# Kernel tuning notes

Hardware: AMD Instinct MI355X
Metric: run time of the kernel (lower is better)

The kernel has to match this reference:

```python
import jax, jax.numpy as jnp
import numpy as np

DELTA = -5.0
DECAY = 0.95
EPS = 1e-05


def setup_inputs() -> dict:
    key = jax.random.key(0)
    k1, k2, k3 = jax.random.split(key, 3)
    N, K, D = 16384, 1024, 256
    z = jax.random.normal(k1, (N, D), dtype=jnp.float32)
    centroids = jax.random.normal(k2, (K, D), dtype=jnp.float32)
    ema_w = jax.random.normal(k3, (K, D), dtype=jnp.float32)
    ema_cluster_size = jnp.ones((K,), dtype=jnp.float32)
    return {"z": z, "centroids": centroids, "ema_w": ema_w,
            "ema_cluster_size": ema_cluster_size}


def reference(z, centroids, ema_w, ema_cluster_size):
    # z: [N, D]; centroids/ema_w: [K, D]; ema_cluster_size: [K]
    K = centroids.shape[0]
    # squared L2 distances via ||z||^2 - 2 z.C^T + ||c||^2 (same math as
    # sum((z[:,None,:]-C)**2, -1), without the (N,K,D) intermediate)
    z_sq = jnp.sum(z * z, axis=1, keepdims=True)          # [N, 1]
    c_sq = jnp.sum(centroids * centroids, axis=1)         # [K]
    z_dist = z_sq - 2.0 * (z @ centroids.T) + c_sq        # [N, K]
    gamma = jax.nn.softmax(DELTA * z_dist, axis=1)        # [N, K]
    idx = jnp.argmax(gamma, axis=1)                       # [N] int
    # recons = one_hot(idx) @ centroids == gather
    recons = centroids[idx]                               # [N, D]
    # --- EMA codebook update (training branch), expressed purely ---
    counts = jnp.zeros((K,), dtype=z.dtype).at[idx].add(jnp.ones((), z.dtype))
    new_cs = ema_cluster_size * DECAY + (1.0 - DECAY) * counts
    n = jnp.sum(new_cs)
    new_cs = (new_cs + EPS) / (n + K * EPS) * n
    dw = jax.ops.segment_sum(z, idx, num_segments=K)      # == Idx.T @ z, [K, D]
    new_w = ema_w * DECAY + (1.0 - DECAY) * dw
    new_centroids = new_w / new_cs[:, None]
    # straight-through estimator
    recons = z + jax.lax.stop_gradient(recons - z)
    return recons, gamma, new_centroids
```

## Files before the change

kernel.cpp:

```cpp
#include <hip/hip_runtime.h>


#define DECAY 0.95f
#define OMD   0.05f
#define EPSV  1e-5f

using i32x4  = __attribute__((ext_vector_type(4))) int;
using i32x16 = __attribute__((ext_vector_type(16))) int;

typedef __attribute__((address_space(3))) unsigned int       lds_uint;
typedef const __attribute__((address_space(1))) unsigned int glb_uint;

__device__ __forceinline__ void gload16(const void* g, const void* l) {
  __builtin_amdgcn_global_load_lds((glb_uint*)(unsigned long long)g,
                                   (lds_uint*)(unsigned int)(unsigned long long)l,
                                   16, 0, 0);
}

__global__ __launch_bounds__(256) void prep(const float* __restrict__ z,
                                            const float* __restrict__ cent,
                                            const float* __restrict__ ema_cs,
                                            signed char* __restrict__ z8,
                                            signed char* __restrict__ c8,
                                            float* __restrict__ sz,
                                            float* __restrict__ sc,
                                            float* __restrict__ csq,
                                            float* __restrict__ dwzero,
                                            float* __restrict__ S) {
  const int bid = blockIdx.x;
  const int t   = threadIdx.x;
  if (bid < 2176) {
    const bool isz = bid < 2048;
    const float* src = isz ? z : cent;
    const int rb = isz ? bid : (bid - 2048);
    const int r  = rb * 8 + (t >> 5);
    const int d0 = (t & 31) * 8;
    const float4 a = *(const float4*)&src[(size_t)r * 256 + d0];
    const float4 b = *(const float4*)&src[(size_t)r * 256 + d0 + 4];
    float f[8] = {a.x, a.y, a.z, a.w, b.x, b.y, b.z, b.w};
    float am = 0.f, ssq = 0.f;
#pragma unroll
    for (int j = 0; j < 8; ++j) { am = fmaxf(am, fabsf(f[j])); ssq += f[j] * f[j]; }
#pragma unroll
    for (int off = 16; off; off >>= 1) {
      am  = fmaxf(am, __shfl_down(am, off, 32));
      ssq += __shfl_down(ssq, off, 32);
    }
    am = __shfl(am, 0, 32);
    const float s  = fmaxf(am, 1e-6f) * (1.0f / 127.0f);
    const float rs = 1.0f / s;
    union { signed char c[8]; uint2 u; } H, L;
#pragma unroll
    for (int j = 0; j < 8; ++j) {
      float q = rintf(f[j] * rs);
      q = fminf(fmaxf(q, -127.f), 127.f);
      H.c[j] = (signed char)(int)q;
      float res = f[j] - q * s;
      float lq = rintf(res * rs * 256.0f);
      lq = fminf(fmaxf(lq, -127.f), 127.f);
      L.c[j] = (signed char)(int)lq;
    }
    signed char* dst = (isz ? z8 : c8) + (size_t)r * 512 + (d0 >> 6) * 128 + (d0 & 63);
    *(uint2*)dst        = H.u;
    *(uint2*)(dst + 64) = L.u;
    if ((t & 31) == 0) {
      if (isz) sz[r] = s;
      else { sc[r] = s; csq[r] = ssq; }
    }
  } else if (bid < 2433) {
    const int i = (bid - 2176) * 256 + t;
    ((float4*)dwzero)[i] = (float4){0.f, 0.f, 0.f, 0.f};
  } else {
    float s = ema_cs[t] + ema_cs[t + 256] + ema_cs[t + 512] + ema_cs[t + 768];
#pragma unroll
    for (int off = 32; off; off >>= 1) s += __shfl_down(s, off);
    __shared__ float wsum[4];
    if ((t & 63) == 0) wsum[t >> 6] = s;
    __syncthreads();
    if (t == 0) S[0] = wsum[0] + wsum[1] + wsum[2] + wsum[3];
  }
}

__global__ __launch_bounds__(256, 2) void dist_gemm_i8(
    const signed char* __restrict__ z8, const signed char* __restrict__ c8,
    const float* __restrict__ sz, const float* __restrict__ sc,
    const float* __restrict__ csq, float* __restrict__ dist) {
  __shared__ signed char lds[2][128 * 128];

  const int tid  = threadIdx.x;
  const int lane = tid & 63;
  const int w    = tid >> 6;

  const int bid = blockIdx.x;
  const int lin = (bid & 7) * 128 + (bid >> 3);
  const int m0  = (lin >> 3) * 128;
  const int n0  = (lin & 7) * 128;

  const int wm0 = (w >> 1) * 64;
  const int wn0 = (w & 1) * 64;

  i32x16 accA[2][2];
  i32x16 accB[2][2];
#pragma unroll
  for (int i = 0; i < 2; ++i)
#pragma unroll
    for (int j = 0; j < 2; ++j) {
      accA[i][j] = (i32x16)(0);
      accB[i][j] = (i32x16)(0);
    }

  const int srow = lane >> 3;
  const int scb  = lane & 7;

  for (int kk = 0; kk < 4; ++kk) {
    __syncthreads();
#pragma unroll
    for (int j = 0; j < 4; ++j) {
      const int r0    = w * 32 + j * 8;
      const int row   = r0 + srow;
      const int chunk = scb ^ (row & 7);
      gload16(z8 + (size_t)(m0 + row) * 512 + kk * 128 + chunk * 16, &lds[0][r0 * 128]);
      gload16(c8 + (size_t)(n0 + row) * 512 + kk * 128 + chunk * 16, &lds[1][r0 * 128]);
    }
    __syncthreads();
#pragma unroll
    for (int s = 0; s < 2; ++s) {
      i32x4 ah[2], al[2], bh[2], bl[2];
      const int kc = s * 2 + (lane >> 5);
#pragma unroll
      for (int fi = 0; fi < 2; ++fi) {
        const int ra = wm0 + fi * 32 + (lane & 31);
        ah[fi] = *(const i32x4*)&lds[0][ra * 128 + ((kc)     ^ (ra & 7)) * 16];
        al[fi] = *(const i32x4*)&lds[0][ra * 128 + ((kc + 4) ^ (ra & 7)) * 16];
        const int rb = wn0 + fi * 32 + (lane & 31);
        bh[fi] = *(const i32x4*)&lds[1][rb * 128 + ((kc)     ^ (rb & 7)) * 16];
        bl[fi] = *(const i32x4*)&lds[1][rb * 128 + ((kc + 4) ^ (rb & 7)) * 16];
      }
#pragma unroll
      for (int i = 0; i < 2; ++i)
#pragma unroll
        for (int j = 0; j < 2; ++j) {
          accA[i][j] = __builtin_amdgcn_mfma_i32_32x32x32_i8(ah[i], bh[j], accA[i][j], 0, 0, 0);
          accB[i][j] = __builtin_amdgcn_mfma_i32_32x32x32_i8(ah[i], bl[j], accB[i][j], 0, 0, 0);
          accB[i][j] = __builtin_amdgcn_mfma_i32_32x32x32_i8(al[i], bh[j], accB[i][j], 0, 0, 0);
        }
    }
  }

#pragma unroll
  for (int j = 0; j < 2; ++j) {
    const int colb = n0 + wn0 + j * 32 + (lane & 31);
    const float scv = sc[colb];
    const float cqv = csq[colb];
#pragma unroll
    for (int i = 0; i < 2; ++i) {
#pragma unroll
      for (int reg = 0; reg < 16; ++reg) {
        const int row = m0 + wm0 + i * 32 + (reg & 3) + 8 * (reg >> 2) + 4 * (lane >> 5);
        const float dotv = (float)accA[i][j][reg] + (float)accB[i][j][reg] * (1.0f / 256.0f);
        dist[(size_t)row * 1024 + colb] = cqv - 2.0f * sz[row] * scv * dotv;
      }
    }
  }
}

__global__ __launch_bounds__(256) void row_softmax(const float* __restrict__ z,
                                                   const float* __restrict__ cent,
                                                   float* __restrict__ gamma,
                                                   float* __restrict__ recons,
                                                   float* __restrict__ dw,
                                                   float* __restrict__ counts,
                                                   int K) {
  const int n = blockIdx.x;
  const int t = threadIdx.x;
  float* row = gamma + (size_t)n * K;
  const float4 s = ((const float4*)row)[t];

  float mv = s.x; int mi = 4 * t;
  if (s.y < mv) { mv = s.y; mi = 4 * t + 1; }
  if (s.z < mv) { mv = s.z; mi = 4 * t + 2; }
  if (s.w < mv) { mv = s.w; mi = 4 * t + 3; }

#pragma unroll
  for (int off = 32; off; off >>= 1) {
    const float ov = __shfl_down(mv, off);
    const int   oi = __shfl_down(mi, off);
    if (ov < mv || (ov == mv && oi < mi)) { mv = ov; mi = oi; }
  }

  __shared__ float wv[4];
  __shared__ int   wi[4];
  __shared__ float fmin_s;
  __shared__ int   fidx_s;
  __shared__ float fsum_s;
  const int wave = t >> 6;
  if ((t & 63) == 0) { wv[wave] = mv; wi[wave] = mi; }
  __syncthreads();
  if (t == 0) {
    float bv = wv[0]; int bi = wi[0];
#pragma unroll
    for (int wq = 1; wq < 4; ++wq)
      if (wv[wq] < bv || (wv[wq] == bv && wi[wq] < bi)) { bv = wv[wq]; bi = wi[wq]; }
    fmin_s = bv; fidx_s = bi;
  }
  __syncthreads();

  const float bm = fmin_s;
  const float e0 = __expf(-5.0f * (s.x - bm));
  const float e1 = __expf(-5.0f * (s.y - bm));
  const float e2 = __expf(-5.0f * (s.z - bm));
  const float e3 = __expf(-5.0f * (s.w - bm));
  float ls = e0 + e1 + e2 + e3;
#pragma unroll
  for (int off = 32; off; off >>= 1) ls += __shfl_down(ls, off);
  if ((t & 63) == 0) wv[wave] = ls;
  __syncthreads();
  if (t == 0) fsum_s = wv[0] + wv[1] + wv[2] + wv[3];
  __syncthreads();

  const float inv = 1.0f / fsum_s;
  float4 g;
  g.x = e0 * inv; g.y = e1 * inv; g.z = e2 * inv; g.w = e3 * inv;
  ((float4*)row)[t] = g;

  const int idx = fidx_s;
  const float zv = z[(size_t)n * 256 + t];
  recons[(size_t)n * 256 + t] = cent[(size_t)idx * 256 + t];
  atomicAdd(&dw[(size_t)idx * 256 + t], zv);
  if (t == 0) atomicAdd(&counts[idx], 1.0f);
}

__global__ __launch_bounds__(256) void finalize(const float* __restrict__ ema_w,
                                                const float* __restrict__ ema_cs,
                                                const float* __restrict__ counts,
                                                const float* __restrict__ dw,
                                                const float* __restrict__ S,
                                                float* __restrict__ outc,
                                                float fN) {
  const int k = blockIdx.x;
  const int t = threadIdx.x;
  const float n   = DECAY * S[0] + OMD * fN;
  const float v   = DECAY * ema_cs[k] + OMD * counts[k];
  const float ncs = (v + EPSV) / (n + 1024.0f * EPSV) * n;
  const size_t i  = (size_t)k * 256 + t;
  outc[i] = (DECAY * ema_w[i] + OMD * dw[i]) / ncs;
}

extern "C" void kernel_launch(void* const* d_in, const int* in_sizes, int n_in,
                              void* d_out, int out_size, void* d_ws, size_t ws_size,
                              hipStream_t stream) {
  const float* z      = (const float*)d_in[0];
  const float* cent   = (const float*)d_in[1];
  const float* ema_w  = (const float*)d_in[2];
  const float* ema_cs = (const float*)d_in[3];

  const int K = in_sizes[3];
  const int D = in_sizes[1] / K;
  const int N = in_sizes[0] / D;

  float* out    = (float*)d_out;
  float* recons = out;
  float* gamma  = out + (size_t)N * D;
  float* outc   = gamma + (size_t)N * K;

  signed char* z8 = (signed char*)recons;
  signed char* c8 = (signed char*)outc;
  float* sz = outc + (size_t)K * 512 / 4;
  float* sc = sz + N;

  float* dw     = (float*)d_ws;
  float* counts = dw + (size_t)K * D;
  float* csq    = counts + K;
  float* S      = csq + K;

  prep<<<2434, 256, 0, stream>>>(z, cent, ema_cs, z8, c8, sz, sc, csq, dw, S);

  dist_gemm_i8<<<(N / 128) * (K / 128), 256, 0, stream>>>(z8, c8, sz, sc, csq, gamma);

  row_softmax<<<N, 256, 0, stream>>>(z, cent, gamma, recons, dw, counts, K);

  finalize<<<K, 256, 0, stream>>>(ema_w, ema_cs, counts, dw, S, outc, (float)N);
}
```

Measured before the change: 77.67 us.

## Fuse z quantization, distance GEMM, softmax and scatter into one kernel

Replaces the separate z-quantization, int8 distance GEMM and row-softmax kernels with one fused kernel per 64-row block. The block quantizes z directly into LDS and runs the GEMM twice over all centroids. The first pass computes per-row min, argmin and partial exp sums, and the second recomputes distances and writes normalized gamma directly. This avoids writing and rereading the full N×K distance matrix and the z8 buffer in global memory, at the cost of doing the GEMM twice. It also drops to 128 blocks of 64 rows, which may limit occupancy and parallelism.

```diff
diff --git a/kernel.cpp b/kernel.cpp
--- a/kernel.cpp
+++ b/kernel.cpp
@@ -17,26 +17,20 @@
                                    16, 0, 0);
 }
 
-__global__ __launch_bounds__(256) void prep(const float* __restrict__ z,
-                                            const float* __restrict__ cent,
+__global__ __launch_bounds__(256) void prep(const float* __restrict__ cent,
                                             const float* __restrict__ ema_cs,
-                                            signed char* __restrict__ z8,
                                             signed char* __restrict__ c8,
-                                            float* __restrict__ sz,
                                             float* __restrict__ sc,
                                             float* __restrict__ csq,
                                             float* __restrict__ dwzero,
                                             float* __restrict__ S) {
   const int bid = blockIdx.x;
   const int t   = threadIdx.x;
-  if (bid < 2176) {
-    const bool isz = bid < 2048;
-    const float* src = isz ? z : cent;
-    const int rb = isz ? bid : (bid - 2048);
-    const int r  = rb * 8 + (t >> 5);
+  if (bid < 128) {
+    const int r  = bid * 8 + (t >> 5);
     const int d0 = (t & 31) * 8;
-    const float4 a = *(const float4*)&src[(size_t)r * 256 + d0];
-    const float4 b = *(const float4*)&src[(size_t)r * 256 + d0 + 4];
+    const float4 a = *(const float4*)&cent[(size_t)r * 256 + d0];
+    const float4 b = *(const float4*)&cent[(size_t)r * 256 + d0 + 4];
     float f[8] = {a.x, a.y, a.z, a.w, b.x, b.y, b.z, b.w};
     float am = 0.f, ssq = 0.f;
 #pragma unroll
@@ -60,15 +54,12 @@
       lq = fminf(fmaxf(lq, -127.f), 127.f);
       L.c[j] = (signed char)(int)lq;
     }
-    signed char* dst = (isz ? z8 : c8) + (size_t)r * 512 + (d0 >> 6) * 128 + (d0 & 63);
+    signed char* dst = c8 + (size_t)r * 512 + (d0 >> 6) * 128 + (d0 & 63);
     *(uint2*)dst        = H.u;
     *(uint2*)(dst + 64) = L.u;
-    if ((t & 31) == 0) {
-      if (isz) sz[r] = s;
-      else { sc[r] = s; csq[r] = ssq; }
-    }
-  } else if (bid < 2433) {
-    const int i = (bid - 2176) * 256 + t;
+    if ((t & 31) == 0) { sc[r] = s; csq[r] = ssq; }
+  } else if (bid < 385) {
+    const int i = (bid - 128) * 256 + t;
     ((float4*)dwzero)[i] = (float4){0.f, 0.f, 0.f, 0.f};
   } else {
     float s = ema_cs[t] + ema_cs[t + 256] + ema_cs[t + 512] + ema_cs[t + 768];
@@ -81,153 +72,186 @@
   }
 }
 
-__global__ __launch_bounds__(256, 2) void dist_gemm_i8(
-    const signed char* __restrict__ z8, const signed char* __restrict__ c8,
-    const float* __restrict__ sz, const float* __restrict__ sc,
-    const float* __restrict__ csq, float* __restrict__ dist) {
-  __shared__ signed char lds[2][128 * 128];
-
-  const int tid  = threadIdx.x;
-  const int lane = tid & 63;
-  const int w    = tid >> 6;
-
-  const int bid = blockIdx.x;
-  const int lin = (bid & 7) * 128 + (bid >> 3);
-  const int m0  = (lin >> 3) * 128;
-  const int n0  = (lin & 7) * 128;
-
-  const int wm0 = (w >> 1) * 64;
-  const int wn0 = (w & 1) * 64;
-
-  i32x16 accA[2][2];
-  i32x16 accB[2][2];
-#pragma unroll
-  for (int i = 0; i < 2; ++i)
-#pragma unroll
-    for (int j = 0; j < 2; ++j) {
-      accA[i][j] = (i32x16)(0);
-      accB[i][j] = (i32x16)(0);
-    }
-
-  const int srow = lane >> 3;
-  const int scb  = lane & 7;
-
-  for (int kk = 0; kk < 4; ++kk) {
-    __syncthreads();
-#pragma unroll
-    for (int j = 0; j < 4; ++j) {
-      const int r0    = w * 32 + j * 8;
-      const int row   = r0 + srow;
-      const int chunk = scb ^ (row & 7);
-      gload16(z8 + (size_t)(m0 + row) * 512 + kk * 128 + chunk * 16, &lds[0][r0 * 128]);
-      gload16(c8 + (size_t)(n0 + row) * 512 + kk * 128 + chunk * 16, &lds[1][r0 * 128]);
-    }
-    __syncthreads();
-#pragma unroll
-    for (int s = 0; s < 2; ++s) {
-      i32x4 ah[2], al[2], bh[2], bl[2];
-      const int kc = s * 2 + (lane >> 5);
-#pragma unroll
-      for (int fi = 0; fi < 2; ++fi) {
-        const int ra = wm0 + fi * 32 + (lane & 31);
-        ah[fi] = *(const i32x4*)&lds[0][ra * 128 + ((kc)     ^ (ra & 7)) * 16];
-        al[fi] = *(const i32x4*)&lds[0][ra * 128 + ((kc + 4) ^ (ra & 7)) * 16];
-        const int rb = wn0 + fi * 32 + (lane & 31);
-        bh[fi] = *(const i32x4*)&lds[1][rb * 128 + ((kc)     ^ (rb & 7)) * 16];
-        bl[fi] = *(const i32x4*)&lds[1][rb * 128 + ((kc + 4) ^ (rb & 7)) * 16];
-      }
-#pragma unroll
-      for (int i = 0; i < 2; ++i)
-#pragma unroll
-        for (int j = 0; j < 2; ++j) {
-          accA[i][j] = __builtin_amdgcn_mfma_i32_32x32x32_i8(ah[i], bh[j], accA[i][j], 0, 0, 0);
-          accB[i][j] = __builtin_amdgcn_mfma_i32_32x32x32_i8(ah[i], bl[j], accB[i][j], 0, 0, 0);
-          accB[i][j] = __builtin_amdgcn_mfma_i32_32x32x32_i8(al[i], bh[j], accB[i][j], 0, 0, 0);
-        }
-    }
-  }
-
-#pragma unroll
-  for (int j = 0; j < 2; ++j) {
-    const int colb = n0 + wn0 + j * 32 + (lane & 31);
-    const float scv = sc[colb];
-    const float cqv = csq[colb];
-#pragma unroll
-    for (int i = 0; i < 2; ++i) {
-#pragma unroll
-      for (int reg = 0; reg < 16; ++reg) {
-        const int row = m0 + wm0 + i * 32 + (reg & 3) + 8 * (reg >> 2) + 4 * (lane >> 5);
-        const float dotv = (float)accA[i][j][reg] + (float)accB[i][j][reg] * (1.0f / 256.0f);
-        dist[(size_t)row * 1024 + colb] = cqv - 2.0f * sz[row] * scv * dotv;
-      }
-    }
-  }
-}
-
-__global__ __launch_bounds__(256) void row_softmax(const float* __restrict__ z,
-                                                   const float* __restrict__ cent,
-                                                   float* __restrict__ gamma,
-                                                   float* __restrict__ recons,
-                                                   float* __restrict__ dw,
-                                                   float* __restrict__ counts,
-                                                   int K) {
-  const int n = blockIdx.x;
-  const int t = threadIdx.x;
-  float* row = gamma + (size_t)n * K;
-  const float4 s = ((const float4*)row)[t];
-
-  float mv = s.x; int mi = 4 * t;
-  if (s.y < mv) { mv = s.y; mi = 4 * t + 1; }
-  if (s.z < mv) { mv = s.z; mi = 4 * t + 2; }
-  if (s.w < mv) { mv = s.w; mi = 4 * t + 3; }
-
-#pragma unroll
-  for (int off = 32; off; off >>= 1) {
-    const float ov = __shfl_down(mv, off);
-    const int   oi = __shfl_down(mi, off);
-    if (ov < mv || (ov == mv && oi < mi)) { mv = ov; mi = oi; }
-  }
-
-  __shared__ float wv[4];
-  __shared__ int   wi[4];
-  __shared__ float fmin_s;
-  __shared__ int   fidx_s;
-  __shared__ float fsum_s;
-  const int wave = t >> 6;
-  if ((t & 63) == 0) { wv[wave] = mv; wi[wave] = mi; }
-  __syncthreads();
-  if (t == 0) {
-    float bv = wv[0]; int bi = wi[0];
-#pragma unroll
-    for (int wq = 1; wq < 4; ++wq)
-      if (wv[wq] < bv || (wv[wq] == bv && wi[wq] < bi)) { bv = wv[wq]; bi = wi[wq]; }
-    fmin_s = bv; fidx_s = bi;
+#define STAGE(u, buf) do {                                                   \
+    const int ct_ = (u) >> 2, kk_ = (u) & 3;                                 \
+    _Pragma("unroll")                                                        \
+    for (int rnd = 0; rnd < 4; ++rnd) {                                      \
+      const int cl_ = w * 32 + rnd * 8 + (lane >> 3);                        \
+      const int p_  = lane & 7;                                              \
+      gload16(c8 + (size_t)(ct_ * 128 + cl_) * 512 + kk_ * 128 +             \
+                  ((p_ ^ (cl_ & 7)) * 16),                                   \
+              &lB[buf][(w * 32 + rnd * 8) * 128]);                           \
+    }                                                                        \
+  } while (0)
+
+__global__ __launch_bounds__(256, 2) void fused_vq(
+    const float* __restrict__ z, const float* __restrict__ cent,
+    const signed char* __restrict__ c8, const float* __restrict__ sc,
+    const float* __restrict__ csq, float* __restrict__ gamma,
+    float* __restrict__ recons, float* __restrict__ dw,
+    float* __restrict__ counts) {
+  __shared__ signed char lA[64 * 512];
+  __shared__ signed char lB[2][128 * 128];
+  __shared__ float sMv[16][64];
+  __shared__ float sSv[16][64];
+  __shared__ int   sIv[16][64];
+  __shared__ float fM[64];
+  __shared__ float fInv[64];
+  __shared__ int   fIdx[64];
+  __shared__ float sZs[64];
+
+  const int t = threadIdx.x, lane = t & 63, w = t >> 6;
+  const int hi = lane >> 5, l31 = lane & 31;
+  const int wr = w >> 1, wc = w & 1;
+  const int m0 = blockIdx.x * 64;
+
+  {
+    const int c  = lane;
+    const int kk = c >> 4, ch = (c & 15) >> 2, jb = (c & 3) * 4;
+#pragma unroll 1
+    for (int it = 0; it < 16; ++it) {
+      const int r = it * 4 + w;
+      const float4 v = *(const float4*)&z[(size_t)(m0 + r) * 256 + c * 4];
+      float am = fmaxf(fmaxf(fabsf(v.x), fabsf(v.y)), fmaxf(fabsf(v.z), fabsf(v.w)));
+#pragma unroll
+      for (int off = 32; off; off >>= 1) am = fmaxf(am, __shfl_xor(am, off));
+      const float s  = fmaxf(am, 1e-6f) * (1.0f / 127.0f);
+      const float rs = 1.0f / s;
+      const float f[4] = {v.x, v.y, v.z, v.w};
+      unsigned int hw = 0, lw = 0;
+#pragma unroll
+      for (int j = 0; j < 4; ++j) {
+        float q = rintf(f[j] * rs);
+        q = fminf(fmaxf(q, -127.f), 127.f);
+        float res = f[j] - q * s;
+        float lq = rintf(res * rs * 256.0f);
+        lq = fminf(fmaxf(lq, -127.f), 127.f);
+        hw |= ((unsigned int)(unsigned char)(signed char)(int)q)  << (8 * j);
+        lw |= ((unsigned int)(unsigned char)(signed char)(int)lq) << (8 * j);
+      }
+      const int haddr = r * 512 + kk * 128 + ((ch ^ (r & 7)) * 16) + jb;
+      *(unsigned int*)&lA[haddr]      = hw;
+      *(unsigned int*)&lA[haddr ^ 64] = lw;
+      if (lane == 0) sZs[r] = s;
+    }
   }
   __syncthreads();
 
-  const float bm = fmin_s;
-  const float e0 = __expf(-5.0f * (s.x - bm));
-  const float e1 = __expf(-5.0f * (s.y - bm));
-  const float e2 = __expf(-5.0f * (s.z - bm));
-  const float e3 = __expf(-5.0f * (s.w - bm));
-  float ls = e0 + e1 + e2 + e3;
-#pragma unroll
-  for (int off = 32; off; off >>= 1) ls += __shfl_down(ls, off);
-  if ((t & 63) == 0) wv[wave] = ls;
-  __syncthreads();
-  if (t == 0) fsum_s = wv[0] + wv[1] + wv[2] + wv[3];
-  __syncthreads();
-
-  const float inv = 1.0f / fsum_s;
-  float4 g;
-  g.x = e0 * inv; g.y = e1 * inv; g.z = e2 * inv; g.w = e3 * inv;
-  ((float4*)row)[t] = g;
-
-  const int idx = fidx_s;
-  const float zv = z[(size_t)n * 256 + t];
-  recons[(size_t)n * 256 + t] = cent[(size_t)idx * 256 + t];
-  atomicAdd(&dw[(size_t)idx * 256 + t], zv);
-  if (t == 0) atomicAdd(&counts[idx], 1.0f);
+  float szv[16];
+#pragma unroll
+  for (int reg = 0; reg < 16; ++reg)
+    szv[reg] = sZs[wr * 32 + (reg & 3) + 8 * (reg >> 2) + 4 * hi];
+
+  const int ra = wr * 32 + l31;
+
+  i32x16 accA[2], accB[2];
+
+#pragma unroll 1
+  for (int pass = 0; pass < 2; ++pass) {
+    STAGE(0, 0);
+#pragma unroll 1
+    for (int u = 0; u < 32; ++u) {
+      const int cur = u & 1;
+      const int ct = u >> 2, kk = u & 3;
+      if (kk == 0) {
+        accA[0] = (i32x16)(0); accA[1] = (i32x16)(0);
+        accB[0] = (i32x16)(0); accB[1] = (i32x16)(0);
+      }
+      __syncthreads();
+      if (u + 1 < 32) STAGE(u + 1, cur ^ 1);
+#pragma unroll
+      for (int s = 0; s < 2; ++s) {
+        const int kc = s * 2 + hi;
+        const i32x4 ah = *(const i32x4*)&lA[ra * 512 + kk * 128 + ((kc ^ (ra & 7)) * 16)];
+        const i32x4 al = *(const i32x4*)&lA[ra * 512 + kk * 128 + (((kc + 4) ^ (ra & 7)) * 16)];
+#pragma unroll
+        for (int fj = 0; fj < 2; ++fj) {
+          const int rb = wc * 64 + fj * 32 + l31;
+          const i32x4 bh = *(const i32x4*)&lB[cur][rb * 128 + ((kc ^ (rb & 7)) * 16)];
+          const i32x4 bl = *(const i32x4*)&lB[cur][rb * 128 + (((kc + 4) ^ (rb & 7)) * 16)];
+          accA[fj] = __builtin_amdgcn_mfma_i32_32x32x32_i8(ah, bh, accA[fj], 0, 0, 0);
+          accB[fj] = __builtin_amdgcn_mfma_i32_32x32x32_i8(ah, bl, accB[fj], 0, 0, 0);
+          accB[fj] = __builtin_amdgcn_mfma_i32_32x32x32_i8(al, bh, accB[fj], 0, 0, 0);
+        }
+      }
+      if (kk == 3) {
+        const int cg0 = ct * 128 + wc * 64 + l31;
+        const float sc0 = sc[cg0],      cq0 = csq[cg0];
+        const float sc1 = sc[cg0 + 32], cq1 = csq[cg0 + 32];
+        if (pass == 0) {
+#pragma unroll
+          for (int reg = 0; reg < 16; ++reg) {
+            const float d0 = (float)accA[0][reg] + (float)accB[0][reg] * (1.0f / 256.0f);
+            const float d1 = (float)accA[1][reg] + (float)accB[1][reg] * (1.0f / 256.0f);
+            const float s0 = cq0 - 2.0f * szv[reg] * sc0 * d0;
+            const float s1 = cq1 - 2.0f * szv[reg] * sc1 * d1;
+            float mv; int mi;
+            if (s1 < s0) { mv = s1; mi = cg0 + 32; } else { mv = s0; mi = cg0; }
+#pragma unroll
+            for (int off = 16; off; off >>= 1) {
+              const float ov = __shfl_xor(mv, off);
+              const int   oi = __shfl_xor(mi, off);
+              if (ov < mv || (ov == mv && oi < mi)) { mv = ov; mi = oi; }
+            }
+            float e = __expf(-5.0f * (s0 - mv)) + __expf(-5.0f * (s1 - mv));
+#pragma unroll
+            for (int off = 16; off; off >>= 1) e += __shfl_xor(e, off);
+            if (l31 == 0) {
+              const int rl = wr * 32 + (reg & 3) + 8 * (reg >> 2) + 4 * hi;
+              sMv[ct * 2 + wc][rl] = mv;
+              sSv[ct * 2 + wc][rl] = e;
+              sIv[ct * 2 + wc][rl] = mi;
+            }
+          }
+        } else {
+#pragma unroll
+          for (int reg = 0; reg < 16; ++reg) {
+            const int rl = wr * 32 + (reg & 3) + 8 * (reg >> 2) + 4 * hi;
+            const float d0 = (float)accA[0][reg] + (float)accB[0][reg] * (1.0f / 256.0f);
+            const float d1 = (float)accA[1][reg] + (float)accB[1][reg] * (1.0f / 256.0f);
+            const float s0 = cq0 - 2.0f * szv[reg] * sc0 * d0;
+            const float s1 = cq1 - 2.0f * szv[reg] * sc1 * d1;
+            const float m = fM[rl], inv = fInv[rl];
+            gamma[(size_t)(m0 + rl) * 1024 + cg0]      = __expf(-5.0f * (s0 - m)) * inv;
+            gamma[(size_t)(m0 + rl) * 1024 + cg0 + 32] = __expf(-5.0f * (s1 - m)) * inv;
+          }
+        }
+      }
+    }
+    if (pass == 0) {
+      __syncthreads();
+      if (t < 64) {
+        float m = 3.0e38f; int mi = 0;
+#pragma unroll
+        for (int e = 0; e < 16; ++e) {
+          const float me = sMv[e][t];
+          if (me < m) { m = me; mi = sIv[e][t]; }
+        }
+        float sum = 0.f;
+#pragma unroll
+        for (int e = 0; e < 16; ++e)
+          sum += sSv[e][t] * __expf(-5.0f * (sMv[e][t] - m));
+        fM[t] = m; fInv[t] = 1.0f / sum; fIdx[t] = mi;
+        atomicAdd(&counts[mi], 1.0f);
+      }
+      __syncthreads();
+    }
+  }
+
+#pragma unroll 1
+  for (int it = 0; it < 16; ++it) {
+    const int r = it * 4 + w;
+    const int n = m0 + r;
+    const int idx = fIdx[r];
+    const float4 zv = *(const float4*)&z[(size_t)n * 256 + lane * 4];
+    const float4 cv = *(const float4*)&cent[(size_t)idx * 256 + lane * 4];
+    *(float4*)&recons[(size_t)n * 256 + lane * 4] = cv;
+    float* dp = &dw[(size_t)idx * 256 + lane * 4];
+    atomicAdd(dp + 0, zv.x);
+    atomicAdd(dp + 1, zv.y);
+    atomicAdd(dp + 2, zv.z);
+    atomicAdd(dp + 3, zv.w);
+  }
 }
 
 __global__ __launch_bounds__(256) void finalize(const float* __restrict__ ema_w,
@@ -263,21 +287,17 @@
   float* gamma  = out + (size_t)N * D;
   float* outc   = gamma + (size_t)N * K;
 
-  signed char* z8 = (signed char*)recons;
   signed char* c8 = (signed char*)outc;
-  float* sz = outc + (size_t)K * 512 / 4;
-  float* sc = sz + N;
+  float* sc = (float*)((char*)outc + (size_t)K * 512);
 
   float* dw     = (float*)d_ws;
   float* counts = dw + (size_t)K * D;
   float* csq    = counts + K;
   float* S      = csq + K;
 
-  prep<<<2434, 256, 0, stream>>>(z, cent, ema_cs, z8, c8, sz, sc, csq, dw, S);
-
-  dist_gemm_i8<<<(N / 128) * (K / 128), 256, 0, stream>>>(z8, c8, sz, sc, csq, gamma);
-
-  row_softmax<<<N, 256, 0, stream>>>(z, cent, gamma, recons, dw, counts, K);
+  prep<<<386, 256, 0, stream>>>(cent, ema_cs, c8, sc, csq, dw, S);
+
+  fused_vq<<<N / 64, 256, 0, stream>>>(z, cent, c8, sc, csq, gamma, recons, dw, counts);
 
   finalize<<<K, 256, 0, stream>>>(ema_w, ema_cs, counts, dw, S, outc, (float)N);
 }
```

After: 285.2 us. 3.67x slower.

## Fuse softmax into int8 distance GEMM using two-pass recompute with partial stats

Applied to the files above, without the earlier changes.

The distance GEMM now runs twice. The first pass produces per-row partial min, argmin and exp-sum statistics for each 64-column slice. A small merge kernel combines these into the final max, the inverse sum and the index. The second pass recomputes the distances and writes the normalized gamma directly. This avoids writing the full NxK distance matrix and reading it back for the row softmax, at the cost of doubling the int8 GEMM compute. Recons gather and dw atomics move to a separate vectorized kernel.

```diff
diff --git a/kernel.cpp b/kernel.cpp
--- a/kernel.cpp
+++ b/kernel.cpp
@@ -81,15 +81,21 @@
   }
 }
 
+template <int PASS>
 __global__ __launch_bounds__(256, 2) void dist_gemm_i8(
     const signed char* __restrict__ z8, const signed char* __restrict__ c8,
     const float* __restrict__ sz, const float* __restrict__ sc,
-    const float* __restrict__ csq, float* __restrict__ dist) {
+    const float* __restrict__ csq,
+    float* __restrict__ sm, float* __restrict__ se, int* __restrict__ si,
+    const float* __restrict__ fM, const float* __restrict__ fInv,
+    float* __restrict__ gamma) {
   __shared__ signed char lds[2][128 * 128];
+  __shared__ float fMl[128], fIl[128];
 
   const int tid  = threadIdx.x;
   const int lane = tid & 63;
   const int w    = tid >> 6;
+  const int hi   = lane >> 5, l31 = lane & 31;
 
   const int bid = blockIdx.x;
   const int lin = (bid & 7) * 128 + (bid >> 3);
@@ -98,16 +104,15 @@
 
   const int wm0 = (w >> 1) * 64;
   const int wn0 = (w & 1) * 64;
-
-  i32x16 accA[2][2];
-  i32x16 accB[2][2];
+  const int wc  = w & 1;
+
+  if (PASS == 1 && tid < 128) { fMl[tid] = fM[m0 + tid]; fIl[tid] = fInv[m0 + tid]; }
+
+  i32x16 accA[2][2], accB[2][2];
 #pragma unroll
   for (int i = 0; i < 2; ++i)
 #pragma unroll
-    for (int j = 0; j < 2; ++j) {
-      accA[i][j] = (i32x16)(0);
-      accB[i][j] = (i32x16)(0);
-    }
+    for (int j = 0; j < 2; ++j) { accA[i][j] = (i32x16)(0); accB[i][j] = (i32x16)(0); }
 
   const int srow = lane >> 3;
   const int scb  = lane & 7;
@@ -126,13 +131,13 @@
 #pragma unroll
     for (int s = 0; s < 2; ++s) {
       i32x4 ah[2], al[2], bh[2], bl[2];
-      const int kc = s * 2 + (lane >> 5);
+      const int kc = s * 2 + hi;
 #pragma unroll
       for (int fi = 0; fi < 2; ++fi) {
-        const int ra = wm0 + fi * 32 + (lane & 31);
+        const int ra = wm0 + fi * 32 + l31;
         ah[fi] = *(const i32x4*)&lds[0][ra * 128 + ((kc)     ^ (ra & 7)) * 16];
         al[fi] = *(const i32x4*)&lds[0][ra * 128 + ((kc + 4) ^ (ra & 7)) * 16];
-        const int rb = wn0 + fi * 32 + (lane & 31);
+        const int rb = wn0 + fi * 32 + l31;
         bh[fi] = *(const i32x4*)&lds[1][rb * 128 + ((kc)     ^ (rb & 7)) * 16];
         bl[fi] = *(const i32x4*)&lds[1][rb * 128 + ((kc + 4) ^ (rb & 7)) * 16];
       }
@@ -147,87 +152,86 @@
     }
   }
 
-#pragma unroll
-  for (int j = 0; j < 2; ++j) {
-    const int colb = n0 + wn0 + j * 32 + (lane & 31);
-    const float scv = sc[colb];
-    const float cqv = csq[colb];
-#pragma unroll
-    for (int i = 0; i < 2; ++i) {
-#pragma unroll
-      for (int reg = 0; reg < 16; ++reg) {
-        const int row = m0 + wm0 + i * 32 + (reg & 3) + 8 * (reg >> 2) + 4 * (lane >> 5);
-        const float dotv = (float)accA[i][j][reg] + (float)accB[i][j][reg] * (1.0f / 256.0f);
-        dist[(size_t)row * 1024 + colb] = cqv - 2.0f * sz[row] * scv * dotv;
+  const int colb = n0 + wn0 + l31;
+  const float sc0 = sc[colb],      cq0 = csq[colb];
+  const float sc1 = sc[colb + 32], cq1 = csq[colb + 32];
+  const int cb16 = (lin & 7) * 2 + wc;
+
+#pragma unroll
+  for (int i = 0; i < 2; ++i) {
+#pragma unroll
+    for (int reg = 0; reg < 16; ++reg) {
+      const int lr = wm0 + i * 32 + (reg & 3) + 8 * (reg >> 2) + 4 * hi;
+      const float szr = sz[m0 + lr];
+      const float d0 = (float)accA[i][0][reg] + (float)accB[i][0][reg] * (1.0f / 256.0f);
+      const float d1 = (float)accA[i][1][reg] + (float)accB[i][1][reg] * (1.0f / 256.0f);
+      const float s0 = cq0 - 2.0f * szr * sc0 * d0;
+      const float s1 = cq1 - 2.0f * szr * sc1 * d1;
+      if (PASS == 0) {
+        float mv; int mi;
+        if (s1 < s0) { mv = s1; mi = colb + 32; } else { mv = s0; mi = colb; }
+#pragma unroll
+        for (int off = 16; off; off >>= 1) {
+          const float ov = __shfl_xor(mv, off);
+          const int   oi = __shfl_xor(mi, off);
+          if (ov < mv || (ov == mv && oi < mi)) { mv = ov; mi = oi; }
+        }
+        float e = __expf(-5.0f * (s0 - mv)) + __expf(-5.0f * (s1 - mv));
+#pragma unroll
+        for (int off = 16; off; off >>= 1) e += __shfl_xor(e, off);
+        if (l31 == 0) {
+          const int gr = cb16 * 16384 + m0 + lr;
+          sm[gr] = mv; se[gr] = e; si[gr] = mi;
+        }
+      } else {
+        const float m = fMl[lr], inv = fIl[lr];
+        float* gp = &gamma[(size_t)(m0 + lr) * 1024];
+        gp[colb]      = __expf(-5.0f * (s0 - m)) * inv;
+        gp[colb + 32] = __expf(-5.0f * (s1 - m)) * inv;
       }
     }
   }
 }
 
-__global__ __launch_bounds__(256) void row_softmax(const float* __restrict__ z,
-                                                   const float* __restrict__ cent,
-                                                   float* __restrict__ gamma,
-                                                   float* __restrict__ recons,
-                                                   float* __restrict__ dw,
-                                                   float* __restrict__ counts,
-                                                   int K) {
-  const int n = blockIdx.x;
-  const int t = threadIdx.x;
-  float* row = gamma + (size_t)n * K;
-  const float4 s = ((const float4*)row)[t];
-
-  float mv = s.x; int mi = 4 * t;
-  if (s.y < mv) { mv = s.y; mi = 4 * t + 1; }
-  if (s.z < mv) { mv = s.z; mi = 4 * t + 2; }
-  if (s.w < mv) { mv = s.w; mi = 4 * t + 3; }
-
-#pragma unroll
-  for (int off = 32; off; off >>= 1) {
-    const float ov = __shfl_down(mv, off);
-    const int   oi = __shfl_down(mi, off);
-    if (ov < mv || (ov == mv && oi < mi)) { mv = ov; mi = oi; }
+__global__ __launch_bounds__(256) void merge_stats(const float* __restrict__ sm,
+                                                   const float* __restrict__ se,
+                                                   const int* __restrict__ si,
+                                                   float* __restrict__ fM,
+                                                   float* __restrict__ fInv,
+                                                   int* __restrict__ fIdx,
+                                                   float* __restrict__ counts) {
+  const int r = blockIdx.x * 256 + threadIdx.x;
+  float m = sm[r]; int mi = si[r];
+#pragma unroll
+  for (int cb = 1; cb < 16; ++cb) {
+    const float mt = sm[cb * 16384 + r];
+    const int   it = si[cb * 16384 + r];
+    if (mt < m || (mt == m && it < mi)) { m = mt; mi = it; }
   }
-
-  __shared__ float wv[4];
-  __shared__ int   wi[4];
-  __shared__ float fmin_s;
-  __shared__ int   fidx_s;
-  __shared__ float fsum_s;
-  const int wave = t >> 6;
-  if ((t & 63) == 0) { wv[wave] = mv; wi[wave] = mi; }
-  __syncthreads();
-  if (t == 0) {
-    float bv = wv[0]; int bi = wi[0];
-#pragma unroll
-    for (int wq = 1; wq < 4; ++wq)
-      if (wv[wq] < bv || (wv[wq] == bv && wi[wq] < bi)) { bv = wv[wq]; bi = wi[wq]; }
-    fmin_s = bv; fidx_s = bi;
-  }
-  __syncthreads();
-
-  const float bm = fmin_s;
-  const float e0 = __expf(-5.0f * (s.x - bm));
-  const float e1 = __expf(-5.0f * (s.y - bm));
-  const float e2 = __expf(-5.0f * (s.z - bm));
-  const float e3 = __expf(-5.0f * (s.w - bm));
-  float ls = e0 + e1 + e2 + e3;
-#pragma unroll
-  for (int off = 32; off; off >>= 1) ls += __shfl_down(ls, off);
-  if ((t & 63) == 0) wv[wave] = ls;
-  __syncthreads();
-  if (t == 0) fsum_s = wv[0] + wv[1] + wv[2] + wv[3];
-  __syncthreads();
-
-  const float inv = 1.0f / fsum_s;
-  float4 g;
-  g.x = e0 * inv; g.y = e1 * inv; g.z = e2 * inv; g.w = e3 * inv;
-  ((float4*)row)[t] = g;
-
-  const int idx = fidx_s;
-  const float zv = z[(size_t)n * 256 + t];
-  recons[(size_t)n * 256 + t] = cent[(size_t)idx * 256 + t];
-  atomicAdd(&dw[(size_t)idx * 256 + t], zv);
-  if (t == 0) atomicAdd(&counts[idx], 1.0f);
+  float sum = 0.f;
+#pragma unroll
+  for (int cb = 0; cb < 16; ++cb)
+    sum += se[cb * 16384 + r] * __expf(-5.0f * (sm[cb * 16384 + r] - m));
+  fM[r] = m; fInv[r] = 1.0f / sum; fIdx[r] = mi;
+  atomicAdd(&counts[mi], 1.0f);
+}
+
+__global__ __launch_bounds__(256) void epi(const float* __restrict__ z,
+                                           const float* __restrict__ cent,
+                                           const int* __restrict__ fIdx,
+                                           float* __restrict__ recons,
+                                           float* __restrict__ dw) {
+  const int r    = blockIdx.x * 4 + (threadIdx.x >> 6);
+  const int lane = threadIdx.x & 63;
+  const int idx  = fIdx[r];
+  const float4 zv = *(const float4*)&z[(size_t)r * 256 + lane * 4];
+  const float4 cv = *(const float4*)&cent[(size_t)idx * 256 + lane * 4];
+  *(float4*)&recons[(size_t)r * 256 + lane * 4] = cv;
+  float* dp = &dw[(size_t)idx * 256 + lane * 4];
+  atomicAdd(dp + 0, zv.x);
+  atomicAdd(dp + 1, zv.y);
+  atomicAdd(dp + 2, zv.z);
+  atomicAdd(dp + 3, zv.w);
 }
 
 __global__ __launch_bounds__(256) void finalize(const float* __restrict__ ema_w,
@@ -264,20 +268,33 @@
   float* outc   = gamma + (size_t)N * K;
 
   signed char* z8 = (signed char*)recons;
+  float* sm = (float*)((char*)recons + (size_t)8 * 1024 * 1024);
+  float* se = sm + 16 * 16384;
+  int*   si = (int*)(se + 16 * 16384);
+
   signed char* c8 = (signed char*)outc;
-  float* sz = outc + (size_t)K * 512 / 4;
+  float* sz = (float*)((char*)outc + (size_t)K * 512);
   float* sc = sz + N;
 
   float* dw     = (float*)d_ws;
   float* counts = dw + (size_t)K * D;
   float* csq    = counts + K;
   float* S      = csq + K;
+  float* fM     = S + 1;
+  float* fInv   = fM + N;
+  int*   fIdx   = (int*)(fInv + N);
 
   prep<<<2434, 256, 0, stream>>>(z, cent, ema_cs, z8, c8, sz, sc, csq, dw, S);
 
-  dist_gemm_i8<<<(N / 128) * (K / 128), 256, 0, stream>>>(z8, c8, sz, sc, csq, gamma);
-
-  row_softmax<<<N, 256, 0, stream>>>(z, cent, gamma, recons, dw, counts, K);
+  dist_gemm_i8<0><<<(N / 128) * (K / 128), 256, 0, stream>>>(
+      z8, c8, sz, sc, csq, sm, se, si, fM, fInv, gamma);
+
+  merge_stats<<<N / 256, 256, 0, stream>>>(sm, se, si, fM, fInv, fIdx, counts);
+
+  dist_gemm_i8<1><<<(N / 128) * (K / 128), 256, 0, stream>>>(
+      z8, c8, sz, sc, csq, sm, se, si, fM, fInv, gamma);
+
+  epi<<<N / 4, 256, 0, stream>>>(z, cent, fIdx, recons, dw);
 
   finalize<<<K, 256, 0, stream>>>(ema_w, ema_cs, counts, dw, S, outc, (float)N);
 }
```

Result: slower. 240.4 us (+209.5%).

## Replace atomic scatter-add of dw with per-centroid gather reduction kernel

Applied to the files above, without the earlier changes.

The softmax kernel now only writes each row's argmax index. A new per-centroid kernel scans all indices with wave ballots, sums the matching z rows, writes recons for those rows, counts members and computes the new centroid in one pass. This removes the float atomicAdds into dw and counts, the dw zeroing pass and the separate finalize kernel. In exchange every one of the K blocks reads the full index array, and work is unbalanced when clusters differ in size.

```diff
diff --git a/kernel.cpp b/kernel.cpp
--- a/kernel.cpp
+++ b/kernel.cpp
@@ -25,7 +25,6 @@
                                             float* __restrict__ sz,
                                             float* __restrict__ sc,
                                             float* __restrict__ csq,
-                                            float* __restrict__ dwzero,
                                             float* __restrict__ S) {
   const int bid = blockIdx.x;
   const int t   = threadIdx.x;
@@ -67,9 +66,6 @@
       if (isz) sz[r] = s;
       else { sc[r] = s; csq[r] = ssq; }
     }
-  } else if (bid < 2433) {
-    const int i = (bid - 2176) * 256 + t;
-    ((float4*)dwzero)[i] = (float4){0.f, 0.f, 0.f, 0.f};
   } else {
     float s = ema_cs[t] + ema_cs[t + 256] + ema_cs[t + 512] + ema_cs[t + 768];
 #pragma unroll
@@ -164,12 +160,8 @@
   }
 }
 
-__global__ __launch_bounds__(256) void row_softmax(const float* __restrict__ z,
-                                                   const float* __restrict__ cent,
-                                                   float* __restrict__ gamma,
-                                                   float* __restrict__ recons,
-                                                   float* __restrict__ dw,
-                                                   float* __restrict__ counts,
+__global__ __launch_bounds__(256) void row_softmax(float* __restrict__ gamma,
+                                                   int* __restrict__ fIdx,
                                                    int K) {
   const int n = blockIdx.x;
   const int t = threadIdx.x;
@@ -191,7 +183,6 @@
   __shared__ float wv[4];
   __shared__ int   wi[4];
   __shared__ float fmin_s;
-  __shared__ int   fidx_s;
   __shared__ float fsum_s;
   const int wave = t >> 6;
   if ((t & 63) == 0) { wv[wave] = mv; wi[wave] = mi; }
@@ -201,7 +192,7 @@
 #pragma unroll
     for (int wq = 1; wq < 4; ++wq)
       if (wv[wq] < bv || (wv[wq] == bv && wi[wq] < bi)) { bv = wv[wq]; bi = wi[wq]; }
-    fmin_s = bv; fidx_s = bi;
+    fmin_s = bv; fIdx[n] = bi;
   }
   __syncthreads();
 
@@ -222,28 +213,68 @@
   float4 g;
   g.x = e0 * inv; g.y = e1 * inv; g.z = e2 * inv; g.w = e3 * inv;
   ((float4*)row)[t] = g;
-
-  const int idx = fidx_s;
-  const float zv = z[(size_t)n * 256 + t];
-  recons[(size_t)n * 256 + t] = cent[(size_t)idx * 256 + t];
-  atomicAdd(&dw[(size_t)idx * 256 + t], zv);
-  if (t == 0) atomicAdd(&counts[idx], 1.0f);
-}
-
-__global__ __launch_bounds__(256) void finalize(const float* __restrict__ ema_w,
-                                                const float* __restrict__ ema_cs,
-                                                const float* __restrict__ counts,
-                                                const float* __restrict__ dw,
-                                                const float* __restrict__ S,
-                                                float* __restrict__ outc,
-                                                float fN) {
-  const int k = blockIdx.x;
-  const int t = threadIdx.x;
-  const float n   = DECAY * S[0] + OMD * fN;
-  const float v   = DECAY * ema_cs[k] + OMD * counts[k];
-  const float ncs = (v + EPSV) / (n + 1024.0f * EPSV) * n;
-  const size_t i  = (size_t)k * 256 + t;
-  outc[i] = (DECAY * ema_w[i] + OMD * dw[i]) / ncs;
+}
+
+__global__ __launch_bounds__(256) void dwfin(const float* __restrict__ z,
+                                             const float* __restrict__ cent,
+                                             const float* __restrict__ ema_w,
+                                             const float* __restrict__ ema_cs,
+                                             const int* __restrict__ fIdx,
+                                             const float* __restrict__ S,
+                                             float* __restrict__ recons,
+                                             float* __restrict__ outc,
+                                             float fN, int N) {
+  __shared__ float part[4][256];
+  __shared__ int scnt[4];
+  const int k    = blockIdx.x;
+  const int w    = threadIdx.x >> 6;
+  const int lane = threadIdx.x & 63;
+  const int Q    = N >> 2;
+
+  const float4 cv = *(const float4*)&cent[(size_t)k * 256 + lane * 4];
+
+  float4 acc = {0.f, 0.f, 0.f, 0.f};
+  int cnt = 0;
+  const int base = w * Q;
+  for (int c = 0; c < Q; c += 64) {
+    const int fi = fIdx[base + c + lane];
+    unsigned long long mask = __ballot(fi == k);
+    cnt += __popcll(mask);
+    while (mask) {
+      const int b = __builtin_ctzll(mask);
+      mask &= mask - 1;
+      const int rr = base + c + b;
+      const float4 zv = *(const float4*)&z[(size_t)rr * 256 + lane * 4];
+      acc.x += zv.x; acc.y += zv.y; acc.z += zv.z; acc.w += zv.w;
+      *(float4*)&recons[(size_t)rr * 256 + lane * 4] = cv;
+    }
+  }
+  *(float4*)&part[w][lane * 4] = acc;
+  if (lane == 0) scnt[w] = cnt;
+  __syncthreads();
+  if (w == 0) {
+    const float4 a0 = *(const float4*)&part[0][lane * 4];
+    const float4 a1 = *(const float4*)&part[1][lane * 4];
+    const float4 a2 = *(const float4*)&part[2][lane * 4];
+    const float4 a3 = *(const float4*)&part[3][lane * 4];
+    float4 tot;
+    tot.x = (a0.x + a1.x) + (a2.x + a3.x);
+    tot.y = (a0.y + a1.y) + (a2.y + a3.y);
+    tot.z = (a0.z + a1.z) + (a2.z + a3.z);
+    tot.w = (a0.w + a1.w) + (a2.w + a3.w);
+    const int  c   = (scnt[0] + scnt[1]) + (scnt[2] + scnt[3]);
+    const float n  = DECAY * S[0] + OMD * fN;
+    const float v  = DECAY * ema_cs[k] + OMD * (float)c;
+    const float ncs = (v + EPSV) / (n + 1024.0f * EPSV) * n;
+    const float rinv = 1.0f / ncs;
+    const float4 w4 = *(const float4*)&ema_w[(size_t)k * 256 + lane * 4];
+    float4 o;
+    o.x = (DECAY * w4.x + OMD * tot.x) * rinv;
+    o.y = (DECAY * w4.y + OMD * tot.y) * rinv;
+    o.z = (DECAY * w4.z + OMD * tot.z) * rinv;
+    o.w = (DECAY * w4.w + OMD * tot.w) * rinv;
+    *(float4*)&outc[(size_t)k * 256 + lane * 4] = o;
+  }
 }
 
 extern "C" void kernel_launch(void* const* d_in, const int* in_sizes, int n_in,
@@ -264,20 +295,21 @@
   float* outc   = gamma + (size_t)N * K;
 
   signed char* z8 = (signed char*)recons;
+
   signed char* c8 = (signed char*)outc;
-  float* sz = outc + (size_t)K * 512 / 4;
+  float* sz = (float*)((char*)outc + (size_t)K * 512);
   float* sc = sz + N;
 
-  float* dw     = (float*)d_ws;
-  float* counts = dw + (size_t)K * D;
-  float* csq    = counts + K;
-  float* S      = csq + K;
-
-  prep<<<2434, 256, 0, stream>>>(z, cent, ema_cs, z8, c8, sz, sc, csq, dw, S);
+  float* csq  = (float*)d_ws;
+  float* S    = csq + K;
+  int*   fIdx = (int*)(S + 1);
+
+  prep<<<2177, 256, 0, stream>>>(z, cent, ema_cs, z8, c8, sz, sc, csq, S);
 
   dist_gemm_i8<<<(N / 128) * (K / 128), 256, 0, stream>>>(z8, c8, sz, sc, csq, gamma);
 
-  row_softmax<<<N, 256, 0, stream>>>(z, cent, gamma, recons, dw, counts, K);
-
-  finalize<<<K, 256, 0, stream>>>(ema_w, ema_cs, counts, dw, S, outc, (float)N);
-}
+  row_softmax<<<N, 256, 0, stream>>>(gamma, fIdx, K);
+
+  dwfin<<<K, 256, 0, stream>>>(z, cent, ema_w, ema_cs, fIdx, S, recons, outc,
+                               (float)N, N);
+}
```

New measurement: 123.5 us. 1.59x slower.
